# Kernel tuning notes

Measured on AMD Instinct MI355X. Metric: run time of the kernel, lower is better.

Reference implementation:

```python
import jax, jax.numpy as jnp
import numpy as np

B, N, D, KG, L = 4, 256, 256, 128, 2
EPS = 1e-5


def setup_inputs() -> dict:
    key = jax.random.key(0)
    ks = jax.random.split(key, 8)
    s = 0.05  # weight init scale
    return {
        "node_feats": jax.random.normal(ks[0], (B, N, D), dtype=jnp.float32),
        "kg_relation_embeddings": jax.random.normal(ks[1], (B, N, N, KG), dtype=jnp.float32),
        "kg_adjacency": jax.random.randint(ks[2], (B, N, N), 0, 2, dtype=jnp.int32),
        # kg_proj: Linear(kg_embed_dim -> node_dim)
        "W_kg": (jax.random.normal(ks[3], (KG, D), dtype=jnp.float32) * s),
        "b_kg": jnp.zeros((D,), dtype=jnp.float32),
        # per-layer MLP: Linear(3D -> D), ReLU, Linear(D -> D); stacked over L layers
        "W1": (jax.random.normal(ks[4], (L, 3 * D, D), dtype=jnp.float32) * s),
        "b1": jnp.zeros((L, D), dtype=jnp.float32),
        "W2": (jax.random.normal(ks[5], (L, D, D), dtype=jnp.float32) * s),
        "b2": jnp.zeros((L, D), dtype=jnp.float32),
        # shared LayerNorm(node_dim)
        "gamma": jnp.ones((D,), dtype=jnp.float32),
        "beta": jnp.zeros((D,), dtype=jnp.float32),
    }


def _layer_norm(x, gamma, beta):
    mu = x.mean(-1, keepdims=True)
    var = ((x - mu) ** 2).mean(-1, keepdims=True)
    return (x - mu) * jax.lax.rsqrt(var + EPS) * gamma + beta


def reference(node_feats, kg_relation_embeddings, kg_adjacency,
              W_kg, b_kg, W1, b1, W2, b2, gamma, beta):
    d = node_feats.shape[-1]
    n_layers = W1.shape[0]
    # kg_proj applied to relation embeddings (same every layer; dropout is eval-mode identity)
    rel_proj = kg_relation_embeddings @ W_kg + b_kg            # (B,N,N,D)
    adj = kg_adjacency[..., None].astype(node_feats.dtype)     # (B,N,N,1)
    h = node_feats
    for l in range(n_layers):
        # split first Linear over the concat [hi, hj, rel_proj] -> avoids building (B,N,N,3D)
        Wa, Wb, Wc = W1[l, :d], W1[l, d:2 * d], W1[l, 2 * d:]
        a = h @ Wa                                             # (B,N,D) contribution of hi
        b = h @ Wb                                             # (B,N,D) contribution of hj
        c = jnp.einsum('bijk,kd->bijd', rel_proj, Wc)          # (B,N,N,D)
        pre = a[:, :, None, :] + b[:, None, :, :] + c + b1[l]  # (B,N,N,D)
        m = jax.nn.relu(pre) @ W2[l] + b2[l]                   # (B,N,N,D)
        msg = (m * adj).sum(axis=2)                            # (B,N,D) sum over source nodes j
        h = _layer_norm(h + msg, gamma, beta)
    return h
```

## Files before the change

### kernel.cpp

```cpp
#include <hip/hip_runtime.h>
#include <hip/hip_bf16.h>

#define B_ 4
#define N_ 256
#define D_ 256
#define KG_ 128
#define EPS_ 1e-5f

typedef __bf16 bf16x8 __attribute__((ext_vector_type(8)));
typedef float  f32x4v __attribute__((ext_vector_type(4)));

__global__ __launch_bounds__(256) void s1_kernel(
    const float* __restrict__ Wkg, const float* __restrict__ W1l,
    const float* __restrict__ bkg, const float* __restrict__ b1l,
    __bf16* __restrict__ WkcT, float* __restrict__ biastot)
{
    const int d = threadIdx.x;
    if (blockIdx.x == KG_) {
        float acc = 0.f;
        for (int k = 0; k < D_; ++k)
            acc += bkg[k] * W1l[(2 * D_ + k) * D_ + d];
        biastot[d] = acc + b1l[d];
        return;
    }
    const int g = blockIdx.x;
    float acc = 0.f;
    for (int k = 0; k < D_; ++k)
        acc += Wkg[g * D_ + k] * W1l[(2 * D_ + k) * D_ + d];
    WkcT[d * KG_ + g] = (__bf16)acc;
}

__global__ __launch_bounds__(256) void s2_kernel(
    const float* __restrict__ hin, const float* __restrict__ W1l,
    const float* __restrict__ biastot,
    float* __restrict__ apb, float* __restrict__ bbout)
{
    __shared__ float hT[D_][4];
    const int tid = threadIdx.x;
    const int R = blockIdx.x * 4;
    {
        const int r = tid & 3, c4 = (tid >> 2) << 2;
        const float4 v = *(const float4*)(hin + (R + r) * D_ + c4);
        hT[c4 + 0][r] = v.x; hT[c4 + 1][r] = v.y;
        hT[c4 + 2][r] = v.z; hT[c4 + 3][r] = v.w;
    }
    __syncthreads();
    float aa[4] = {0.f, 0.f, 0.f, 0.f};
    float ab[4] = {0.f, 0.f, 0.f, 0.f};
#pragma unroll 4
    for (int e = 0; e < D_; ++e) {
        const float wa = W1l[e * D_ + tid];
        const float wb = W1l[(D_ + e) * D_ + tid];
        const float4 hv = *(const float4*)&hT[e][0];
        aa[0] += hv.x * wa; aa[1] += hv.y * wa; aa[2] += hv.z * wa; aa[3] += hv.w * wa;
        ab[0] += hv.x * wb; ab[1] += hv.y * wb; ab[2] += hv.z * wb; ab[3] += hv.w * wb;
    }
    const float bt = biastot[tid];
#pragma unroll
    for (int r = 0; r < 4; ++r) {
        apb[(R + r) * D_ + tid]   = aa[r] + bt;
        bbout[(R + r) * D_ + tid] = ab[r];
    }
}

__global__ __launch_bounds__(256, 3) void big_kernel(
    const float* __restrict__ rel, const int* __restrict__ adj,
    const __bf16* __restrict__ WkcT, const float* __restrict__ apb,
    const float* __restrict__ bb, const float* __restrict__ W2l,
    const float* __restrict__ b2l, const float* __restrict__ hin,
    const float* __restrict__ gmm, const float* __restrict__ bta,
    float* __restrict__ hout)
{
    __shared__ __align__(16) __bf16 Et[2][16 * KG_];
    __shared__ float bbL[2][16][D_ + 4];
    __shared__ float adjL[N_];
    __shared__ float rL[D_];
    __shared__ float red[8];
    __shared__ float sdeg;

    const int tid = threadIdx.x;
    const int lane = tid & 63;
    const int w = tid >> 6;
    const int l15 = lane & 15;
    const int lg = lane >> 4;
    const int bi = blockIdx.x;
    const int dw = w * 64;

    const float* Ebase  = rel + (size_t)bi * N_ * KG_;
    const float* bbBase = bb + (size_t)(bi >> 8) * N_ * D_;

    bf16x8 wf[4][4];
#pragma unroll
    for (int nb = 0; nb < 4; ++nb)
#pragma unroll
        for (int kk = 0; kk < 4; ++kk)
            wf[nb][kk] = *(const bf16x8*)(WkcT + (dw + nb * 16 + l15) * KG_ + kk * 32 + lg * 8);

    float apbv[4];
#pragma unroll
    for (int nb = 0; nb < 4; ++nb)
        apbv[nb] = apb[bi * D_ + dw + nb * 16 + l15];

    adjL[tid] = (float)adj[bi * N_ + tid];

    float racc[4] = {0.f, 0.f, 0.f, 0.f};

    auto stage = [&](int jb, int buf) {
        const int jp = tid >> 4;
        const int k0 = (tid & 15) * 8;
        const float* src = Ebase + (jb * 16 + jp) * KG_ + k0;
        const float4 f0 = *(const float4*)src;
        const float4 f1 = *(const float4*)(src + 4);
        bf16x8 v;
        v[0] = (__bf16)f0.x; v[1] = (__bf16)f0.y; v[2] = (__bf16)f0.z; v[3] = (__bf16)f0.w;
        v[4] = (__bf16)f1.x; v[5] = (__bf16)f1.y; v[6] = (__bf16)f1.z; v[7] = (__bf16)f1.w;
        int off = jp * 256 + k0 * 2;
        off ^= (jp & 7) << 4;
        *(bf16x8*)((char*)&Et[buf][0] + off) = v;
#pragma unroll
        for (int c = 0; c < 4; ++c) {
            const int flat = tid + c * 256;
            const int row = flat >> 6;
            const int c4 = (flat & 63) * 4;
            *(float4*)&bbL[buf][row][c4] = *(const float4*)(bbBase + (jb * 16 + row) * D_ + c4);
        }
    };

    stage(0, 0);
    __syncthreads();

#pragma unroll 2
    for (int jb = 0; jb < 16; ++jb) {
        const int buf = jb & 1;
        if (jb + 1 < 16) stage(jb + 1, buf ^ 1);

        bf16x8 af[4];
#pragma unroll
        for (int kk = 0; kk < 4; ++kk) {
            int off = l15 * 256 + kk * 64 + lg * 16;
            off ^= (l15 & 7) << 4;
            af[kk] = *(const bf16x8*)((const char*)&Et[buf][0] + off);
        }
#pragma unroll
        for (int nb = 0; nb < 4; ++nb) {
            f32x4v acc = {0.f, 0.f, 0.f, 0.f};
#pragma unroll
            for (int kk = 0; kk < 4; ++kk)
                acc = __builtin_amdgcn_mfma_f32_16x16x32_bf16(af[kk], wf[nb][kk], acc, 0, 0, 0);
#pragma unroll
            for (int q = 0; q < 4; ++q) {
                const int jl = lg * 4 + q;
                float t = acc[q] + apbv[nb] + bbL[buf][jl][dw + nb * 16 + l15];
                t = fmaxf(t, 0.f);
                racc[nb] += t * adjL[jb * 16 + jl];
            }
        }
        __syncthreads();
    }

#pragma unroll
    for (int nb = 0; nb < 4; ++nb) {
        float v = racc[nb];
        v += __shfl_xor(v, 16, 64);
        v += __shfl_xor(v, 32, 64);
        if (lg == 0) rL[dw + nb * 16 + l15] = v;
    }
    if (w == 0) {
        float s = adjL[lane] + adjL[lane + 64] + adjL[lane + 128] + adjL[lane + 192];
#pragma unroll
        for (int off = 32; off >= 1; off >>= 1) s += __shfl_xor(s, off, 64);
        if (lane == 0) sdeg = s;
    }
    __syncthreads();

    const int d = tid;
    float m0 = 0.f, m1 = 0.f, m2 = 0.f, m3 = 0.f;
    for (int e = 0; e < D_; e += 4) {
        const float4 rv = *(const float4*)&rL[e];
        m0 += rv.x * W2l[(e + 0) * D_ + d];
        m1 += rv.y * W2l[(e + 1) * D_ + d];
        m2 += rv.z * W2l[(e + 2) * D_ + d];
        m3 += rv.w * W2l[(e + 3) * D_ + d];
    }
    const float t = hin[bi * D_ + d] + (m0 + m1) + (m2 + m3) + sdeg * b2l[d];

    float s = t, sq = t * t;
#pragma unroll
    for (int off = 32; off >= 1; off >>= 1) {
        s  += __shfl_xor(s, off, 64);
        sq += __shfl_xor(sq, off, 64);
    }
    if (lane == 0) { red[w] = s; red[4 + w] = sq; }
    __syncthreads();
    const float S  = red[0] + red[1] + red[2] + red[3];
    const float SQ = red[4] + red[5] + red[6] + red[7];
    const float mu = S * (1.f / D_);
    const float var = SQ * (1.f / D_) - mu * mu;
    const float rstd = rsqrtf(var + EPS_);
    hout[bi * D_ + d] = (t - mu) * rstd * gmm[d] + bta[d];
}

extern "C" void kernel_launch(void* const* d_in, const int* in_sizes, int n_in,
                              void* d_out, int out_size, void* d_ws, size_t ws_size,
                              hipStream_t stream)
{
    const float* node  = (const float*)d_in[0];
    const float* rel   = (const float*)d_in[1];
    const int*   adj   = (const int*)d_in[2];
    const float* Wkg   = (const float*)d_in[3];
    const float* bkg   = (const float*)d_in[4];
    const float* W1    = (const float*)d_in[5];
    const float* b1    = (const float*)d_in[6];
    const float* W2    = (const float*)d_in[7];
    const float* b2    = (const float*)d_in[8];
    const float* gamma = (const float*)d_in[9];
    const float* beta  = (const float*)d_in[10];
    float* out = (float*)d_out;

    char* ws = (char*)d_ws;
    float*  h1    = (float*)(ws);
    float*  apb   = (float*)(ws + (1 << 20));
    float*  bbuf  = (float*)(ws + (2 << 20));
    float*  bias  = (float*)(ws + (3 << 20));
    __bf16* WkcT  = (__bf16*)(ws + (3 << 20) + 4096);

    for (int l = 0; l < 2; ++l) {
        const float* W1l = W1 + (size_t)l * 3 * D_ * D_;
        const float* hin = (l == 0) ? node : h1;
        float* hout = (l == 1) ? out : h1;

        s1_kernel<<<KG_ + 1, 256, 0, stream>>>(Wkg, W1l, bkg, b1 + l * D_, WkcT, bias);
        s2_kernel<<<(B_ * N_) / 4, 256, 0, stream>>>(hin, W1l, bias, apb, bbuf);
        big_kernel<<<B_ * N_, 256, 0, stream>>>(rel, adj, WkcT, apb, bbuf,
                                                W2 + (size_t)l * D_ * D_, b2 + l * D_,
                                                hin, gamma, beta, hout);
    }
}
```

Measured before the change: 220.9 us.

## Store bb in bf16 and stage it via async global-to-LDS loads

The per-node b projection is now written in bf16 and staged into shared memory with direct global_load_lds 16-byte transfers, using an XOR-swizzled layout. This halves its LDS footprint and removes the register round trip. The smaller shared memory allows raising the occupancy hint from 3 to 4 blocks per CU, and the MFMA loop is reordered so each A fragment feeds all four N-blocks. Storing b in bf16 lowers precision of the pre-activation term, and the async LDS load relies on the existing barrier for ordering.

```diff
diff --git a/kernel.cpp b/kernel.cpp
--- a/kernel.cpp
+++ b/kernel.cpp
@@ -9,6 +9,12 @@
 
 typedef __bf16 bf16x8 __attribute__((ext_vector_type(8)));
 typedef float  f32x4v __attribute__((ext_vector_type(4)));
+
+__device__ __forceinline__ void gload16(const void* g, void* l) {
+    __builtin_amdgcn_global_load_lds(
+        (const __attribute__((address_space(1))) uint32_t*)g,
+        (__attribute__((address_space(3))) uint32_t*)l, 16, 0, 0);
+}
 
 __global__ __launch_bounds__(256) void s1_kernel(
     const float* __restrict__ Wkg, const float* __restrict__ W1l,
@@ -33,7 +39,7 @@
 __global__ __launch_bounds__(256) void s2_kernel(
     const float* __restrict__ hin, const float* __restrict__ W1l,
     const float* __restrict__ biastot,
-    float* __restrict__ apb, float* __restrict__ bbout)
+    float* __restrict__ apb, __bf16* __restrict__ bbout)
 {
     __shared__ float hT[D_][4];
     const int tid = threadIdx.x;
@@ -58,21 +64,21 @@
     const float bt = biastot[tid];
 #pragma unroll
     for (int r = 0; r < 4; ++r) {
-        apb[(R + r) * D_ + tid]   = aa[r] + bt;
-        bbout[(R + r) * D_ + tid] = ab[r];
-    }
-}
-
-__global__ __launch_bounds__(256, 3) void big_kernel(
+        apb[(R + r) * D_ + tid]    = aa[r] + bt;
+        bbout[(R + r) * D_ + tid]  = (__bf16)ab[r];
+    }
+}
+
+__global__ __launch_bounds__(256, 4) void big_kernel(
     const float* __restrict__ rel, const int* __restrict__ adj,
     const __bf16* __restrict__ WkcT, const float* __restrict__ apb,
-    const float* __restrict__ bb, const float* __restrict__ W2l,
+    const __bf16* __restrict__ bb, const float* __restrict__ W2l,
     const float* __restrict__ b2l, const float* __restrict__ hin,
     const float* __restrict__ gmm, const float* __restrict__ bta,
     float* __restrict__ hout)
 {
     __shared__ __align__(16) __bf16 Et[2][16 * KG_];
-    __shared__ float bbL[2][16][D_ + 4];
+    __shared__ __align__(16) __bf16 Bt[2][16 * D_];
     __shared__ float adjL[N_];
     __shared__ float rL[D_];
     __shared__ float red[8];
@@ -86,8 +92,8 @@
     const int bi = blockIdx.x;
     const int dw = w * 64;
 
-    const float* Ebase  = rel + (size_t)bi * N_ * KG_;
-    const float* bbBase = bb + (size_t)(bi >> 8) * N_ * D_;
+    const float*  Ebase  = rel + (size_t)bi * N_ * KG_;
+    const __bf16* bbBase = bb + (size_t)(bi >> 8) * N_ * D_;
 
     bf16x8 wf[4][4];
 #pragma unroll
@@ -105,7 +111,7 @@
 
     float racc[4] = {0.f, 0.f, 0.f, 0.f};
 
-    auto stage = [&](int jb, int buf) {
+    auto stageE = [&](int jb, int buf) {
         const int jp = tid >> 4;
         const int k0 = (tid & 15) * 8;
         const float* src = Ebase + (jb * 16 + jp) * KG_ + k0;
@@ -117,42 +123,54 @@
         int off = jp * 256 + k0 * 2;
         off ^= (jp & 7) << 4;
         *(bf16x8*)((char*)&Et[buf][0] + off) = v;
-#pragma unroll
-        for (int c = 0; c < 4; ++c) {
-            const int flat = tid + c * 256;
-            const int row = flat >> 6;
-            const int c4 = (flat & 63) * 4;
-            *(float4*)&bbL[buf][row][c4] = *(const float4*)(bbBase + (jb * 16 + row) * D_ + c4);
+    };
+
+    auto stageB = [&](int jb, int buf) {
+        const __bf16* Gb = bbBase + jb * 16 * D_;
+        char* ldsbase = (char*)&Bt[buf][0] + (tid & 0xC0) * 16;
+#pragma unroll
+        for (int i = 0; i < 2; ++i) {
+            const int u = tid + i * 256;
+            const int gu = (u & ~31) | ((u & 31) ^ ((u >> 7) & 3));
+            gload16(Gb + gu * 8, ldsbase + i * 256 * 16);
         }
     };
 
-    stage(0, 0);
+    stageE(0, 0);
+    stageB(0, 0);
     __syncthreads();
 
 #pragma unroll 2
     for (int jb = 0; jb < 16; ++jb) {
         const int buf = jb & 1;
-        if (jb + 1 < 16) stage(jb + 1, buf ^ 1);
-
-        bf16x8 af[4];
+        if (jb + 1 < 16) { stageE(jb + 1, buf ^ 1); stageB(jb + 1, buf ^ 1); }
+
+        f32x4v acc[4];
+#pragma unroll
+        for (int nb = 0; nb < 4; ++nb) acc[nb] = (f32x4v){0.f, 0.f, 0.f, 0.f};
+
 #pragma unroll
         for (int kk = 0; kk < 4; ++kk) {
             int off = l15 * 256 + kk * 64 + lg * 16;
             off ^= (l15 & 7) << 4;
-            af[kk] = *(const bf16x8*)((const char*)&Et[buf][0] + off);
+            const bf16x8 af = *(const bf16x8*)((const char*)&Et[buf][0] + off);
+#pragma unroll
+            for (int nb = 0; nb < 4; ++nb)
+                acc[nb] = __builtin_amdgcn_mfma_f32_16x16x32_bf16(af, wf[nb][kk], acc[nb], 0, 0, 0);
         }
-#pragma unroll
-        for (int nb = 0; nb < 4; ++nb) {
-            f32x4v acc = {0.f, 0.f, 0.f, 0.f};
-#pragma unroll
-            for (int kk = 0; kk < 4; ++kk)
-                acc = __builtin_amdgcn_mfma_f32_16x16x32_bf16(af[kk], wf[nb][kk], acc, 0, 0, 0);
-#pragma unroll
-            for (int q = 0; q < 4; ++q) {
-                const int jl = lg * 4 + q;
-                float t = acc[q] + apbv[nb] + bbL[buf][jl][dw + nb * 16 + l15];
+
+#pragma unroll
+        for (int q = 0; q < 4; ++q) {
+            const int jl = lg * 4 + q;
+            const float aj = adjL[jb * 16 + jl];
+#pragma unroll
+            for (int nb = 0; nb < 4; ++nb) {
+                const int d = dw + nb * 16 + l15;
+                const int u = jl * 32 + ((d >> 3) ^ (jl >> 2));
+                const float bv = (float)Bt[buf][u * 8 + (d & 7)];
+                float t = acc[nb][q] + apbv[nb] + bv;
                 t = fmaxf(t, 0.f);
-                racc[nb] += t * adjL[jb * 16 + jl];
+                racc[nb] += t * aj;
             }
         }
         __syncthreads();
@@ -220,7 +238,7 @@
     char* ws = (char*)d_ws;
     float*  h1    = (float*)(ws);
     float*  apb   = (float*)(ws + (1 << 20));
-    float*  bbuf  = (float*)(ws + (2 << 20));
+    __bf16* bbuf  = (__bf16*)(ws + (2 << 20));
     float*  bias  = (float*)(ws + (3 << 20));
     __bf16* WkcT  = (__bf16*)(ws + (3 << 20) + 4096);
 
```

New measurement: 235.7 us. +6.7%, slower.
